# Optimization experiments

Hardware: AMD Instinct MI355X
Metric: run time of the kernel (lower is better)

## Reference

```python
import jax, jax.numpy as jnp
import numpy as np

D_MODEL = 1024
D_INNER = 2048        # expand=2
D_STATE = 128
NHEADS = 16           # d_inner / headdim
HEADDIM = 128
D_CONV = 4
D_XBC = D_INNER + 2 * D_STATE          # 2304 (ngroups=1)
D_IN_PROJ = 2 * D_INNER + 2 * D_STATE + NHEADS  # 4368
BATCH, SEQLEN = 2, 2048
EPS = 1e-5


def setup_inputs() -> dict:
    key = jax.random.key(0)
    ks = jax.random.split(key, 8)
    f = jnp.float32
    return {
        "x": jax.random.normal(ks[0], (BATCH, SEQLEN, D_MODEL), f),
        "ln_w": jnp.ones((D_MODEL,), f),
        "ln_b": jnp.zeros((D_MODEL,), f),
        "W_in": jax.random.normal(ks[1], (D_MODEL, D_IN_PROJ), f) * 0.02,
        "conv_w": jax.random.normal(ks[2], (D_XBC, D_CONV), f) * 0.2,
        "conv_b": jnp.zeros((D_XBC,), f),
        "dt_bias": jax.random.uniform(ks[3], (NHEADS,), f, -4.0, -2.0),
        "A_log": jnp.log(jax.random.uniform(ks[4], (NHEADS,), f, 1.0, 16.0)),
        "D": jnp.ones((NHEADS,), f),
        "rms_w": jnp.ones((D_INNER,), f),
        "W_out": jax.random.normal(ks[5], (D_INNER, D_MODEL), f) * 0.02,
    }


def _mamba_wrap(x, ln_w, ln_b, W_in, conv_w, conv_b, dt_bias, A_log, D, rms_w, W_out):
    B, L = x.shape[0], x.shape[1]
    # LayerNorm (pre-norm)
    mu = jnp.mean(x, -1, keepdims=True)
    var = jnp.mean(jnp.square(x - mu), -1, keepdims=True)
    xn = (x - mu) * jax.lax.rsqrt(var + EPS) * ln_w + ln_b
    # input projection -> z, xBC, dt
    zxbcdt = xn @ W_in                               # (B,L,4368)
    z = zxbcdt[..., :D_INNER]                        # (B,L,2048)
    xBC = zxbcdt[..., D_INNER:D_INNER + D_XBC]       # (B,L,2304)
    dt = jax.nn.softplus(zxbcdt[..., -NHEADS:] + dt_bias)  # (B,L,16)
    # causal depthwise conv1d (kernel 4), then SiLU
    xp = jnp.pad(xBC, ((0, 0), (D_CONV - 1, 0), (0, 0)))
    taps = jnp.stack([xp[:, k:k + L, :] for k in range(D_CONV)], axis=-1)  # (B,L,C,K)
    xBC = jax.nn.silu(jnp.einsum('blck,ck->blc', taps, conv_w) + conv_b)
    # split into SSM inputs
    xh = xBC[..., :D_INNER].reshape(B, L, NHEADS, HEADDIM)   # (B,L,H,P)
    Bm = xBC[..., D_INNER:D_INNER + D_STATE]                  # (B,L,N) ngroups=1
    Cm = xBC[..., D_INNER + D_STATE:]                         # (B,L,N)
    A = -jnp.exp(A_log)                                       # (H,)
    dA = jnp.exp(dt * A)                                      # (B,L,H)

    def step(state, inp):
        xt, dtt, dAt, Bt, Ct = inp  # (B,H,P),(B,H),(B,H),(B,N),(B,N)
        state = state * dAt[..., None, None] + (dtt[..., None] * xt)[..., None] * Bt[:, None, None, :]
        y = jnp.einsum('bhpn,bn->bhp', state, Ct)
        return state, y

    init = jnp.zeros((B, NHEADS, HEADDIM, D_STATE), x.dtype)
    xs = (xh.transpose(1, 0, 2, 3), dt.transpose(1, 0, 2), dA.transpose(1, 0, 2),
          Bm.transpose(1, 0, 2), Cm.transpose(1, 0, 2))
    _, ys = jax.lax.scan(step, init, xs)                      # (L,B,H,P)
    y = ys.transpose(1, 0, 2, 3) + D[None, None, :, None] * xh  # skip term
    y = y.reshape(B, L, D_INNER)
    # gated RMSNorm: rmsnorm(y * silu(z)) * weight
    y = y * jax.nn.silu(z)
    y = y * jax.lax.rsqrt(jnp.mean(y * y, -1, keepdims=True) + EPS) * rms_w
    # output projection + residual
    return x + y @ W_out


def reference(x, ln_w, ln_b, W_in, conv_w, conv_b, dt_bias, A_log, D, rms_w, W_out):
    return _mamba_wrap(x, ln_w, ln_b, W_in, conv_w, conv_b, dt_bias, A_log, D, rms_w, W_out)
```

## Files before the change

### kernel.cpp

```cpp
#include <hip/hip_runtime.h>

typedef unsigned short ushort_t;
typedef __attribute__((ext_vector_type(8))) unsigned short ushort8;
typedef __attribute__((ext_vector_type(4))) unsigned short ushortv4;
typedef __attribute__((ext_vector_type(8))) __bf16 bf16x8;
typedef __attribute__((ext_vector_type(4))) float f32x4;

#define BATCH   2
#define SEQLEN  2048
#define BL      4096
#define DMODEL  1024
#define DINNER  2048
#define DSTATE  128
#define NHEADS  16
#define DXBC    2304
#define DPROJ   4368
#define NPAD    4480
#define EPSF    1e-5f
#define QCH     128
#define NCH     16
#define BH      32

#define SWZ(row, colbyte) ((colbyte) ^ (((row) & 7) << 4))

#define GLDS(gp, lp) __builtin_amdgcn_global_load_lds( \
    (const __attribute__((address_space(1))) void*)(gp), \
    (__attribute__((address_space(3))) void*)(lp), 16, 0, 0)

__device__ __forceinline__ float bf2f(ushort_t h) {
    unsigned int u = ((unsigned int)h) << 16;
    float f; __builtin_memcpy(&f, &u, 4); return f;
}
__device__ __forceinline__ ushort_t f2bf(float f) {
    unsigned int u; __builtin_memcpy(&u, &f, 4);
    unsigned int r = u + 0x7fffu + ((u >> 16) & 1u);
    return (ushort_t)(r >> 16);
}
__device__ __forceinline__ float siluf(float x) { return x / (1.f + expf(-x)); }
__device__ __forceinline__ float softplusf(float x) { return (x > 20.f) ? x : log1pf(expf(x)); }

__global__ __launch_bounds__(256) void ln_kernel(const float* __restrict__ x,
        const float* __restrict__ w, const float* __restrict__ b, ushort_t* __restrict__ xn) {
    int r = blockIdx.x, t = threadIdx.x;
    const float* xr = x + (size_t)r * DMODEL;
    float4 v = *(const float4*)&xr[t * 4];
    float s  = v.x + v.y + v.z + v.w;
    float sq = v.x*v.x + v.y*v.y + v.z*v.z + v.w*v.w;
    __shared__ float red[8];
    #pragma unroll
    for (int m = 32; m >= 1; m >>= 1) { s += __shfl_xor(s, m, 64); sq += __shfl_xor(sq, m, 64); }
    int wv = t >> 6;
    if ((t & 63) == 0) { red[wv] = s; red[4 + wv] = sq; }
    __syncthreads();
    s  = red[0] + red[1] + red[2] + red[3];
    sq = red[4] + red[5] + red[6] + red[7];
    float mu  = s * (1.f / DMODEL);
    float var = sq * (1.f / DMODEL) - mu * mu;
    float inv = rsqrtf(var + EPSF);
    float4 wv4 = *(const float4*)&w[t * 4];
    float4 bv4 = *(const float4*)&b[t * 4];
    ushortv4 o;
    o[0] = f2bf((v.x - mu) * inv * wv4.x + bv4.x);
    o[1] = f2bf((v.y - mu) * inv * wv4.y + bv4.y);
    o[2] = f2bf((v.z - mu) * inv * wv4.z + bv4.z);
    o[3] = f2bf((v.w - mu) * inv * wv4.w + bv4.w);
    *(ushortv4*)&xn[(size_t)r * DMODEL + t * 4] = o;
}

__global__ __launch_bounds__(256) void transpose_cast(const float* __restrict__ W,
        ushort_t* __restrict__ WT, int K, int N) {
    __shared__ float tile[32][33];
    int n0 = blockIdx.x * 32, k0 = blockIdx.y * 32;
    int tx = threadIdx.x & 31, ty = threadIdx.x >> 5;
    #pragma unroll
    for (int i = 0; i < 32; i += 8) {
        int n = n0 + tx;
        tile[ty + i][tx] = (n < N) ? W[(size_t)(k0 + ty + i) * N + n] : 0.f;
    }
    __syncthreads();
    #pragma unroll
    for (int i = 0; i < 32; i += 8) {
        WT[(size_t)(n0 + ty + i) * K + k0 + tx] = f2bf(tile[tx][ty + i]);
    }
}

__global__ __launch_bounds__(256) void convw_tr(const float* __restrict__ w,
        float* __restrict__ wt) {
    int c = blockIdx.x * 256 + threadIdx.x;
    if (c < DXBC) {
        float4 v = *(const float4*)&w[c * 4];
        wt[0 * DXBC + c] = v.x;
        wt[1 * DXBC + c] = v.y;
        wt[2 * DXBC + c] = v.z;
        wt[3 * DXBC + c] = v.w;
    }
}

template <bool OUTBF>
__global__ __launch_bounds__(256) void gemm_bt(const ushort_t* __restrict__ A,
        const ushort_t* __restrict__ BT, void* __restrict__ Cv,
        const float* __restrict__ resid, int K, int ldc, int nbx) {
    const int tid = threadIdx.x;
    const int nwg = gridDim.x;
    const int cpx = nwg >> 3;
    const int lid = (blockIdx.x & 7) * cpx + (blockIdx.x >> 3);
    const int m0 = (lid / nbx) * 128, n0 = (lid % nbx) * 128;
    __shared__ ushort_t As[2][128 * 32];
    __shared__ ushort_t Bs[2][128 * 32];
    const int lane = tid & 63, wave = tid >> 6;
    const int wrow = wave * 32;
    const int srow = lane >> 2;
    const int selm = (lane & 3) * 8;
    const ushort_t* ag0 = A  + (size_t)(m0 + wrow + srow) * K + selm;
    const ushort_t* ag1 = ag0 + (size_t)16 * K;
    const ushort_t* bg0 = BT + (size_t)(n0 + wrow + srow) * K + selm;
    const ushort_t* bg1 = bg0 + (size_t)16 * K;
    const int wm = (wave >> 1) * 64, wn = (wave & 1) * 64;
    const int fr = lane & 15, ko = (lane >> 4) * 8;
    f32x4 acc[4][4];
    #pragma unroll
    for (int i = 0; i < 4; i++)
        #pragma unroll
        for (int j = 0; j < 4; j++) acc[i][j] = (f32x4){0.f, 0.f, 0.f, 0.f};
    GLDS(ag0, &As[0][wrow * 32]);
    GLDS(ag1, &As[0][(wrow + 16) * 32]);
    GLDS(bg0, &Bs[0][wrow * 32]);
    GLDS(bg1, &Bs[0][(wrow + 16) * 32]);
    __syncthreads();
    int cur = 0;
    for (int k0 = 0; k0 < K; k0 += 32) {
        const int nxt = cur ^ 1;
        if (k0 + 32 < K) {
            GLDS(ag0 + k0 + 32, &As[nxt][wrow * 32]);
            GLDS(ag1 + k0 + 32, &As[nxt][(wrow + 16) * 32]);
            GLDS(bg0 + k0 + 32, &Bs[nxt][wrow * 32]);
            GLDS(bg1 + k0 + 32, &Bs[nxt][(wrow + 16) * 32]);
        }
        bf16x8 af[4], bfr[4];
        #pragma unroll
        for (int i = 0; i < 4; i++) af[i]  = *(const bf16x8*)&As[cur][(wm + i * 16 + fr) * 32 + ko];
        #pragma unroll
        for (int j = 0; j < 4; j++) bfr[j] = *(const bf16x8*)&Bs[cur][(wn + j * 16 + fr) * 32 + ko];
        #pragma unroll
        for (int i = 0; i < 4; i++)
            #pragma unroll
            for (int j = 0; j < 4; j++)
                acc[i][j] = __builtin_amdgcn_mfma_f32_16x16x32_bf16(af[i], bfr[j], acc[i][j], 0, 0, 0);
        __syncthreads();
        cur = nxt;
    }
    const int r0 = (lane >> 4) * 4;
    #pragma unroll
    for (int i = 0; i < 4; i++)
        #pragma unroll
        for (int j = 0; j < 4; j++)
            #pragma unroll
            for (int r = 0; r < 4; r++) {
                int m = m0 + wm + i * 16 + r0 + r;
                int n = n0 + wn + j * 16 + fr;
                float v = acc[i][j][r];
                if (OUTBF) {
                    ((ushort_t*)Cv)[(size_t)m * ldc + n] = f2bf(v);
                } else {
                    if (resid) v += resid[(size_t)m * ldc + n];
                    ((float*)Cv)[(size_t)m * ldc + n] = v;
                }
            }
}

__global__ __launch_bounds__(256) void conv_kernel(const ushort_t* __restrict__ zxb,
        const float* __restrict__ wtr, const float* __restrict__ conv_b,
        const float* __restrict__ dt_bias, const float* __restrict__ A_log,
        ushort_t* __restrict__ xcv, ushort_t* __restrict__ Bcg, ushort_t* __restrict__ Ccg,
        float* __restrict__ dtv, float* __restrict__ dta) {
    int bid = blockIdx.x;
    int l = bid & (SEQLEN - 1);
    int tid = threadIdx.x;
    const ushort_t* rowp = zxb + (size_t)bid * NPAD;
    #pragma unroll 1
    for (int u = tid; u < DXBC / 8; u += 256) {
        int c0 = u * 8;
        float acc[8];
        {
            float4 b0 = *(const float4*)&conv_b[c0];
            float4 b1 = *(const float4*)&conv_b[c0 + 4];
            acc[0] = b0.x; acc[1] = b0.y; acc[2] = b0.z; acc[3] = b0.w;
            acc[4] = b1.x; acc[5] = b1.y; acc[6] = b1.z; acc[7] = b1.w;
        }
        #pragma unroll
        for (int k = 0; k < 4; k++) {
            int ll = l - 3 + k;
            if (ll >= 0) {
                ushort8 xv = *(const ushort8*)&rowp[(ptrdiff_t)(k - 3) * NPAD + DINNER + c0];
                float4 w0 = *(const float4*)&wtr[k * DXBC + c0];
                float4 w1 = *(const float4*)&wtr[k * DXBC + c0 + 4];
                acc[0] += bf2f((ushort_t)xv[0]) * w0.x;
                acc[1] += bf2f((ushort_t)xv[1]) * w0.y;
                acc[2] += bf2f((ushort_t)xv[2]) * w0.z;
                acc[3] += bf2f((ushort_t)xv[3]) * w0.w;
                acc[4] += bf2f((ushort_t)xv[4]) * w1.x;
                acc[5] += bf2f((ushort_t)xv[5]) * w1.y;
                acc[6] += bf2f((ushort_t)xv[6]) * w1.z;
                acc[7] += bf2f((ushort_t)xv[7]) * w1.w;
            }
        }
        ushort8 o;
        #pragma unroll
        for (int e = 0; e < 8; e++) o[e] = f2bf(siluf(acc[e]));
        if (c0 < DINNER)                *(ushort8*)&xcv[(size_t)bid * DINNER + c0] = o;
        else if (c0 < DINNER + DSTATE)  *(ushort8*)&Bcg[(size_t)bid * DSTATE + (c0 - DINNER)] = o;
        else                            *(ushort8*)&Ccg[(size_t)bid * DSTATE + (c0 - DINNER - DSTATE)] = o;
    }
    if (tid < NHEADS) {
        float raw = bf2f(rowp[DINNER + DXBC + tid]) + dt_bias[tid];
        float dt = softplusf(raw);
        float A = -expf(A_log[tid]);
        dtv[(size_t)bid * NHEADS + tid] = dt;
        dta[(size_t)bid * NHEADS + tid] = dt * A;
    }
}

__global__ __launch_bounds__(128) void cumsum_kernel(const float* __restrict__ dta,
        const float* __restrict__ dtv, float* __restrict__ cabuf, float* __restrict__ expca,
        float* __restrict__ wbuf, float* __restrict__ dtbuf, float* __restrict__ dtot) {
    const int c = blockIdx.x, h = blockIdx.y, b = blockIdx.z;
    const int bh = b * NHEADS + h;
    const int j = threadIdx.x;
    const size_t row = (size_t)b * SEQLEN + c * QCH + j;
    float v  = dta[row * NHEADS + h];
    float dt = dtv[row * NHEADS + h];
    float pv = v;
    #pragma unroll
    for (int off = 1; off < 64; off <<= 1) {
        float u = __shfl_up(pv, off, 64);
        if ((j & 63) >= off) pv += u;
    }
    __shared__ float wsum[2];
    if ((j & 63) == 63) wsum[j >> 6] = pv;
    __syncthreads();
    float tot = wsum[0] + wsum[1];
    if (j >= 64) pv += wsum[0];
    const size_t idx = ((size_t)bh * NCH + c) * QCH + j;
    cabuf[idx] = pv;
    expca[idx] = expf(pv);
    wbuf[idx]  = expf(tot - pv) * dt;
    dtbuf[idx] = dt;
    if (j == 0) dtot[bh * NCH + c] = expf(tot);
}

__global__ __launch_bounds__(256) void chunkstate_kernel(const ushort_t* __restrict__ xcv,
        const ushort_t* __restrict__ Bcg, const float* __restrict__ wbuf,
        ushort_t* __restrict__ states) {
    const int c = blockIdx.x, h = blockIdx.y, b = blockIdx.z;
    const int bh = b * NHEADS + h;
    const int tid = threadIdx.x;
    __shared__ ushort_t Xt[128 * 128];
    __shared__ ushort_t Bt[128 * 128];
    __shared__ float wsh[QCH];
    if (tid < QCH) wsh[tid] = wbuf[((size_t)bh * NCH + c) * QCH + tid];
    __syncthreads();
    const size_t row0 = (size_t)b * SEQLEN + c * QCH;
    {
        const int f = tid & 127;
        const int jh = (tid >> 7) * 64;
        const ushort_t* xsrc = xcv + (row0 + jh) * DINNER + h * 128 + f;
        const ushort_t* bsrc = Bcg + (row0 + jh) * DSTATE + f;
        char* xrow = (char*)Xt + f * 256;
        char* brow = (char*)Bt + f * 256;
        #pragma unroll 2
        for (int e8 = 0; e8 < 8; e8++) {
            ushort8 tx, tb;
            #pragma unroll
            for (int e = 0; e < 8; e++) {
                int j = e8 * 8 + e;
                tx[e] = xsrc[(size_t)j * DINNER];
                tb[e] = f2bf(bf2f(bsrc[(size_t)j * DSTATE]) * wsh[jh + j]);
            }
            int cb = (jh + e8 * 8) * 2;
            *(ushort8*)(xrow + SWZ(f, cb)) = tx;
            *(ushort8*)(brow + SWZ(f, cb)) = tb;
        }
    }
    __syncthreads();
    const int lane = tid & 63, wave = tid >> 6;
    const int wp = (wave >> 1) * 64, wn = (wave & 1) * 64;
    const int fr = lane & 15, ko = (lane >> 4) * 8;
    f32x4 acc[4][4];
    #pragma unroll
    for (int i = 0; i < 4; i++)
        #pragma unroll
        for (int j = 0; j < 4; j++) acc[i][j] = (f32x4){0.f, 0.f, 0.f, 0.f};
    for (int k0 = 0; k0 < 128; k0 += 32) {
        bf16x8 af[4], bfr[4];
        #pragma unroll
        for (int i = 0; i < 4; i++) {
            int rp = wp + i * 16 + fr;
            af[i] = *(const bf16x8*)((const char*)Xt + rp * 256 + SWZ(rp, (k0 + ko) * 2));
        }
        #pragma unroll
        for (int j = 0; j < 4; j++) {
            int rn = wn + j * 16 + fr;
            bfr[j] = *(const bf16x8*)((const char*)Bt + rn * 256 + SWZ(rn, (k0 + ko) * 2));
        }
        #pragma unroll
        for (int i = 0; i < 4; i++)
            #pragma unroll
            for (int j = 0; j < 4; j++)
                acc[i][j] = __builtin_amdgcn_mfma_f32_16x16x32_bf16(af[i], bfr[j], acc[i][j], 0, 0, 0);
    }
    const int r0 = (lane >> 4) * 4;
    ushort_t* outp = states + ((size_t)bh * NCH + c) * 16384;
    #pragma unroll
    for (int i = 0; i < 4; i++)
        #pragma unroll
        for (int j = 0; j < 4; j++)
            #pragma unroll
            for (int r = 0; r < 4; r++)
                outp[(wp + i * 16 + r0 + r) * 128 + wn + j * 16 + fr] = f2bf(acc[i][j][r]);
}

__global__ __launch_bounds__(256) void statescan_kernel(ushort_t* __restrict__ states,
        const float* __restrict__ dtot) {
    const int pseg = blockIdx.x, bh = blockIdx.y;
    const int tid = threadIdx.x;
    const int p = pseg * 8 + (tid >> 5);
    const int n4 = (tid & 31) * 4;
    ushort_t* base = states + (size_t)bh * NCH * 16384 + p * 128 + n4;
    const float* dtp = dtot + bh * NCH;
    float r0 = 0.f, r1 = 0.f, r2 = 0.f, r3 = 0.f;
    #pragma unroll 1
    for (int c = 0; c < NCH; c++) {
        ushortv4* ptr = (ushortv4*)(base + (size_t)c * 16384);
        ushortv4 cs = *ptr;
        ushortv4 o;
        o[0] = f2bf(r0); o[1] = f2bf(r1); o[2] = f2bf(r2); o[3] = f2bf(r3);
        *ptr = o;
        float d = dtp[c];
        r0 = r0 * d + bf2f(cs[0]);
        r1 = r1 * d + bf2f(cs[1]);
        r2 = r2 * d + bf2f(cs[2]);
        r3 = r3 * d + bf2f(cs[3]);
    }
}

__global__ __launch_bounds__(256) void chunkout_kernel(const ushort_t* __restrict__ xcv,
        const ushort_t* __restrict__ Bcg, const ushort_t* __restrict__ Ccg,
        const ushort_t* __restrict__ states, const float* __restrict__ cabuf,
        const float* __restrict__ expca, const float* __restrict__ dtbuf,
        const float* __restrict__ Dvec, ushort_t* __restrict__ yv) {
    const int c = blockIdx.x, h = blockIdx.y, b = blockIdx.z;
    const int bh = b * NHEADS + h;
    const int tid = threadIdx.x;
    __shared__ ushort_t R1[128 * 128];
    __shared__ ushort_t R2[128 * 128];
    __shared__ float cash[QCH], dtsh[QCH], exsh[QCH];
    const size_t aidx = ((size_t)bh * NCH + c) * QCH;
    if (tid < QCH) {
        cash[tid] = cabuf[aidx + tid];
        dtsh[tid] = dtbuf[aidx + tid];
        exsh[tid] = expca[aidx + tid];
    }
    const size_t row0 = (size_t)b * SEQLEN + c * QCH;
    {
        const ushort_t* sp = states + ((size_t)bh * NCH + c) * 16384;
        #pragma unroll
        for (int it = 0; it < 8; it++) {
            int g = tid + it * 256;
            int r = g >> 4, n8 = (g & 15) * 8;
            ushort8 vc = *(const ushort8*)&Ccg[(row0 + r) * DSTATE + n8];
            ushort8 vs = *(const ushort8*)&sp[r * 128 + n8];
            int cb = n8 * 2;
            *(ushort8*)((char*)R2 + r * 256 + SWZ(r, cb)) = vc;
            *(ushort8*)((char*)R1 + r * 256 + SWZ(r, cb)) = vs;
        }
    }
    __syncthreads();
    const int lane = tid & 63, wave = tid >> 6;
    const int fr = lane & 15, ko = (lane >> 4) * 8, r0 = (lane >> 4) * 4;
    const int wty = (wave >> 1) * 64, wpy = (wave & 1) * 64;
    f32x4 y_[4][4];
    #pragma unroll
    for (int i = 0; i < 4; i++)
        #pragma unroll
        for (int j = 0; j < 4; j++) y_[i][j] = (f32x4){0.f, 0.f, 0.f, 0.f};
    for (int k0 = 0; k0 < 128; k0 += 32) {
        bf16x8 af[4], bfr[4];
        #pragma unroll
        for (int i = 0; i < 4; i++) {
            int rt = wty + i * 16 + fr;
            af[i] = *(const bf16x8*)((const char*)R2 + rt * 256 + SWZ(rt, (k0 + ko) * 2));
        }
        #pragma unroll
        for (int j = 0; j < 4; j++) {
            int rp = wpy + j * 16 + fr;
            bfr[j] = *(const bf16x8*)((const char*)R1 + rp * 256 + SWZ(rp, (k0 + ko) * 2));
        }
        #pragma unroll
        for (int i = 0; i < 4; i++)
            #pragma unroll
            for (int j = 0; j < 4; j++)
                y_[i][j] = __builtin_amdgcn_mfma_f32_16x16x32_bf16(af[i], bfr[j], y_[i][j], 0, 0, 0);
    }
    #pragma unroll
    for (int i = 0; i < 4; i++)
        #pragma unroll
        for (int r = 0; r < 4; r++) {
            float sc = exsh[wty + i * 16 + r0 + r];
            #pragma unroll
            for (int j = 0; j < 4; j++) y_[i][j][r] *= sc;
        }
    __syncthreads();
    #pragma unroll
    for (int it = 0; it < 8; it++) {
        int g = tid + it * 256;
        int r = g >> 4, n8 = (g & 15) * 8;
        ushort8 vb = *(const ushort8*)&Bcg[(row0 + r) * DSTATE + n8];
        *(ushort8*)((char*)R1 + r * 256 + SWZ(r, n8 * 2)) = vb;
    }
    __syncthreads();
    const int wj = (wave >> 1) * 64, wt = (wave & 1) * 64;
    f32x4 g_[4][4];
    #pragma unroll
    for (int i = 0; i < 4; i++)
        #pragma unroll
        for (int t = 0; t < 4; t++) g_[i][t] = (f32x4){0.f, 0.f, 0.f, 0.f};
    if (!(wj == 64 && wt == 0)) {
        for (int k0 = 0; k0 < 128; k0 += 32) {
            bf16x8 af[4], bfr[4];
            #pragma unroll
            for (int i = 0; i < 4; i++) {
                int rj = wj + i * 16 + fr;
                af[i] = *(const bf16x8*)((const char*)R1 + rj * 256 + SWZ(rj, (k0 + ko) * 2));
            }
            #pragma unroll
            for (int t = 0; t < 4; t++) {
                int rt = wt + t * 16 + fr;
                bfr[t] = *(const bf16x8*)((const char*)R2 + rt * 256 + SWZ(rt, (k0 + ko) * 2));
            }
            #pragma unroll
            for (int i = 0; i < 4; i++)
                #pragma unroll
                for (int t = 0; t < 4; t++)
                    g_[i][t] = __builtin_amdgcn_mfma_f32_16x16x32_bf16(af[i], bfr[t], g_[i][t], 0, 0, 0);
        }
    }
    __syncthreads();
    {
        const float Dh = Dvec[h];
        #pragma unroll
        for (int i = 0; i < 4; i++) {
            #pragma unroll
            for (int t = 0; t < 4; t++) {
                int tt = wt + t * 16 + fr;
                int jj0 = wj + i * 16 + r0;
                ushortv4 pk;
                #pragma unroll
                for (int r = 0; r < 4; r++) {
                    int jj = jj0 + r;
                    float val = 0.f;
                    if (jj <= tt) {
                        val = g_[i][t][r] * expf(cash[tt] - cash[jj]) * dtsh[jj];
                        if (jj == tt) val += Dh;
                    }
                    pk[r] = f2bf(val);
                }
                *(ushortv4*)((char*)R1 + tt * 256 + SWZ(tt, jj0 * 2)) = pk;
            }
        }
        const int f = tid & 127;
        const int jh = (tid >> 7) * 64;
        const ushort_t* xsrc = xcv + (row0 + jh) * DINNER + h * 128 + f;
        char* xrow = (char*)R2 + f * 256;
        #pragma unroll 2
        for (int e8 = 0; e8 < 8; e8++) {
            ushort8 tx;
            #pragma unroll
            for (int e = 0; e < 8; e++) tx[e] = xsrc[(size_t)(e8 * 8 + e) * DINNER];
            int cb = (jh + e8 * 8) * 2;
            *(ushort8*)(xrow + SWZ(f, cb)) = tx;
        }
    }
    __syncthreads();
    const int kmax = wty + 64;
    for (int k0 = 0; k0 < kmax; k0 += 32) {
        bf16x8 af[4], bfr[4];
        #pragma unroll
        for (int i = 0; i < 4; i++) {
            int rt = wty + i * 16 + fr;
            af[i] = *(const bf16x8*)((const char*)R1 + rt * 256 + SWZ(rt, (k0 + ko) * 2));
        }
        #pragma unroll
        for (int j = 0; j < 4; j++) {
            int rp = wpy + j * 16 + fr;
            bfr[j] = *(const bf16x8*)((const char*)R2 + rp * 256 + SWZ(rp, (k0 + ko) * 2));
        }
        #pragma unroll
        for (int i = 0; i < 4; i++)
            #pragma unroll
            for (int j = 0; j < 4; j++)
                y_[i][j] = __builtin_amdgcn_mfma_f32_16x16x32_bf16(af[i], bfr[j], y_[i][j], 0, 0, 0);
    }
    #pragma unroll
    for (int i = 0; i < 4; i++)
        #pragma unroll
        for (int j = 0; j < 4; j++)
            #pragma unroll
            for (int r = 0; r < 4; r++) {
                int t = wty + i * 16 + r0 + r;
                int p = wpy + j * 16 + fr;
                yv[(row0 + t) * DINNER + h * 128 + p] = f2bf(y_[i][j][r]);
            }
}

__global__ __launch_bounds__(256) void gate_rms(const ushort_t* __restrict__ yv,
        const ushort_t* __restrict__ zxb, const float* __restrict__ rms_w,
        ushort_t* __restrict__ ynorm) {
    int r = blockIdx.x, t = threadIdx.x;
    const ushort_t* yr = yv + (size_t)r * DINNER;
    const ushort_t* zr = zxb + (size_t)r * NPAD;
    ushort8 y8 = *(const ushort8*)&yr[t * 8];
    ushort8 z8 = *(const ushort8*)&zr[t * 8];
    float g[8];
    #pragma unroll
    for (int j = 0; j < 8; j++)
        g[j] = bf2f((ushort_t)y8[j]) * siluf(bf2f((ushort_t)z8[j]));
    float sq = 0.f;
    #pragma unroll
    for (int j = 0; j < 8; j++) sq += g[j] * g[j];
    __shared__ float red[4];
    #pragma unroll
    for (int m = 32; m >= 1; m >>= 1) sq += __shfl_xor(sq, m, 64);
    int wv = t >> 6;
    if ((t & 63) == 0) red[wv] = sq;
    __syncthreads();
    sq = red[0] + red[1] + red[2] + red[3];
    float scale = rsqrtf(sq * (1.f / DINNER) + EPSF);
    float4 w0 = *(const float4*)&rms_w[t * 8];
    float4 w1 = *(const float4*)&rms_w[t * 8 + 4];
    ushort8 o;
    o[0] = f2bf(g[0] * scale * w0.x);
    o[1] = f2bf(g[1] * scale * w0.y);
    o[2] = f2bf(g[2] * scale * w0.z);
    o[3] = f2bf(g[3] * scale * w0.w);
    o[4] = f2bf(g[4] * scale * w1.x);
    o[5] = f2bf(g[5] * scale * w1.y);
    o[6] = f2bf(g[6] * scale * w1.z);
    o[7] = f2bf(g[7] * scale * w1.w);
    *(ushort8*)&ynorm[(size_t)r * DINNER + t * 8] = o;
}

extern "C" void kernel_launch(void* const* d_in, const int* in_sizes, int n_in,
                              void* d_out, int out_size, void* d_ws, size_t ws_size,
                              hipStream_t stream) {
    (void)in_sizes; (void)n_in; (void)out_size; (void)ws_size;
    const float* x       = (const float*)d_in[0];
    const float* ln_w    = (const float*)d_in[1];
    const float* ln_b    = (const float*)d_in[2];
    const float* W_in    = (const float*)d_in[3];
    const float* conv_w  = (const float*)d_in[4];
    const float* conv_b  = (const float*)d_in[5];
    const float* dt_bias = (const float*)d_in[6];
    const float* A_log   = (const float*)d_in[7];
    const float* Dvec    = (const float*)d_in[8];
    const float* rms_w   = (const float*)d_in[9];
    const float* W_out   = (const float*)d_in[10];
    float* out = (float*)d_out;

    char* ws = (char*)d_ws;
    size_t off = 0;
    auto alloc = [&](size_t bytes) -> void* {
        void* p = ws + off;
        off += (bytes + 255) & ~(size_t)255;
        return p;
    };
    ushort_t* xn    = (ushort_t*)alloc((size_t)BL * DMODEL * 2);
    ushort_t* WinT  = (ushort_t*)alloc((size_t)NPAD * DMODEL * 2);
    ushort_t* zxb   = (ushort_t*)alloc((size_t)BL * NPAD * 2);
    ushort_t* xcv   = (ushort_t*)alloc((size_t)BL * DINNER * 2);
    ushort_t* Bcg   = (ushort_t*)alloc((size_t)BL * DSTATE * 2);
    ushort_t* Ccg   = (ushort_t*)alloc((size_t)BL * DSTATE * 2);
    float*    dtv   = (float*)   alloc((size_t)BL * NHEADS * 4);
    float*    dta   = (float*)   alloc((size_t)BL * NHEADS * 4);
    ushort_t* yv    = (ushort_t*)alloc((size_t)BL * DINNER * 2);
    ushort_t* ynorm = (ushort_t*)alloc((size_t)BL * DINNER * 2);
    ushort_t* WoutT = (ushort_t*)alloc((size_t)DMODEL * DINNER * 2);
    float*    wtr   = (float*)   alloc((size_t)4 * DXBC * 4);
    float*    cabuf = (float*)   alloc((size_t)BH * NCH * QCH * 4);
    float*    expcb = (float*)   alloc((size_t)BH * NCH * QCH * 4);
    float*    wbuf  = (float*)   alloc((size_t)BH * NCH * QCH * 4);
    float*    dtbuf = (float*)   alloc((size_t)BH * NCH * QCH * 4);
    float*    dtot  = (float*)   alloc((size_t)BH * NCH * 4);
    ushort_t* states= (ushort_t*)alloc((size_t)BH * NCH * 16384 * 2);

    ln_kernel<<<BL, 256, 0, stream>>>(x, ln_w, ln_b, xn);
    transpose_cast<<<dim3(NPAD / 32, DMODEL / 32), 256, 0, stream>>>(W_in, WinT, DMODEL, DPROJ);
    transpose_cast<<<dim3(DMODEL / 32, DINNER / 32), 256, 0, stream>>>(W_out, WoutT, DINNER, DMODEL);
    convw_tr<<<(DXBC + 255) / 256, 256, 0, stream>>>(conv_w, wtr);
    gemm_bt<true><<<(NPAD / 128) * (BL / 128), 256, 0, stream>>>(xn, WinT, zxb, nullptr, DMODEL, NPAD, NPAD / 128);
    conv_kernel<<<BL, 256, 0, stream>>>(zxb, wtr, conv_b, dt_bias, A_log, xcv, Bcg, Ccg, dtv, dta);
    cumsum_kernel<<<dim3(NCH, NHEADS, BATCH), 128, 0, stream>>>(dta, dtv, cabuf, expcb, wbuf, dtbuf, dtot);
    chunkstate_kernel<<<dim3(NCH, NHEADS, BATCH), 256, 0, stream>>>(xcv, Bcg, wbuf, states);
    statescan_kernel<<<dim3(16, BH), 256, 0, stream>>>(states, dtot);
    chunkout_kernel<<<dim3(NCH, NHEADS, BATCH), 256, 0, stream>>>(xcv, Bcg, Ccg, states, cabuf, expcb, dtbuf, Dvec, yv);
    gate_rms<<<BL, 256, 0, stream>>>(yv, zxb, rms_w, ynorm);
    gemm_bt<false><<<(DMODEL / 128) * (BL / 128), 256, 0, stream>>>(ynorm, WoutT, out, x, DINNER, DMODEL, DMODEL / 128);
}
```

Baseline: 205.8 us.

## Triple-buffer GEMM LDS tiles with fine-grained vmcnt waits and XOR swizzle

The bf16 GEMM moves from double to triple buffering of the global-to-LDS tiles, prefetching two K-steps ahead. The full __syncthreads is replaced by explicit s_waitcnt vmcnt counts plus s_barrier, so loads for later tiles can stay in flight across iterations. The global source column is also XOR-swizzled by row, and the LDS reads un-swizzle to match, to cut LDS bank conflicts on the fragment reads. This costs extra LDS per block, which may lower occupancy, and relies on hand-counted vmcnt values being correct.

Measured after the change: 208.3 us. About the same (+1.2%).

```diff
diff --git a/kernel.cpp b/kernel.cpp
--- a/kernel.cpp
+++ b/kernel.cpp
@@ -105,12 +105,12 @@
     const int cpx = nwg >> 3;
     const int lid = (blockIdx.x & 7) * cpx + (blockIdx.x >> 3);
     const int m0 = (lid / nbx) * 128, n0 = (lid % nbx) * 128;
-    __shared__ ushort_t As[2][128 * 32];
-    __shared__ ushort_t Bs[2][128 * 32];
+    __shared__ ushort_t As[3][128 * 32];
+    __shared__ ushort_t Bs[3][128 * 32];
     const int lane = tid & 63, wave = tid >> 6;
     const int wrow = wave * 32;
     const int srow = lane >> 2;
-    const int selm = (lane & 3) * 8;
+    const int selm = ((lane & 3) ^ (srow & 3)) * 8;
     const ushort_t* ag0 = A  + (size_t)(m0 + wrow + srow) * K + selm;
     const ushort_t* ag1 = ag0 + (size_t)16 * K;
     const ushort_t* bg0 = BT + (size_t)(n0 + wrow + srow) * K + selm;
@@ -122,32 +122,49 @@
     for (int i = 0; i < 4; i++)
         #pragma unroll
         for (int j = 0; j < 4; j++) acc[i][j] = (f32x4){0.f, 0.f, 0.f, 0.f};
-    GLDS(ag0, &As[0][wrow * 32]);
-    GLDS(ag1, &As[0][(wrow + 16) * 32]);
-    GLDS(bg0, &Bs[0][wrow * 32]);
-    GLDS(bg1, &Bs[0][(wrow + 16) * 32]);
-    __syncthreads();
+    const int nt = K >> 5;
+    #pragma unroll
+    for (int t = 0; t < 3; t++) {
+        const size_t kof = (size_t)t * 32;
+        GLDS(ag0 + kof, &As[t][wrow * 32]);
+        GLDS(ag1 + kof, &As[t][(wrow + 16) * 32]);
+        GLDS(bg0 + kof, &Bs[t][wrow * 32]);
+        GLDS(bg1 + kof, &Bs[t][(wrow + 16) * 32]);
+    }
+    asm volatile("s_waitcnt vmcnt(8)" ::: "memory");
+    __builtin_amdgcn_s_barrier();
     int cur = 0;
-    for (int k0 = 0; k0 < K; k0 += 32) {
-        const int nxt = cur ^ 1;
-        if (k0 + 32 < K) {
-            GLDS(ag0 + k0 + 32, &As[nxt][wrow * 32]);
-            GLDS(ag1 + k0 + 32, &As[nxt][(wrow + 16) * 32]);
-            GLDS(bg0 + k0 + 32, &Bs[nxt][wrow * 32]);
-            GLDS(bg1 + k0 + 32, &Bs[nxt][(wrow + 16) * 32]);
+    for (int t = 0; t < nt; ++t) {
+        if (t + 2 < nt) {
+            int nb = cur + 2; if (nb >= 3) nb -= 3;
+            const size_t kof = (size_t)(t + 2) * 32;
+            GLDS(ag0 + kof, &As[nb][wrow * 32]);
+            GLDS(ag1 + kof, &As[nb][(wrow + 16) * 32]);
+            GLDS(bg0 + kof, &Bs[nb][wrow * 32]);
+            GLDS(bg1 + kof, &Bs[nb][(wrow + 16) * 32]);
         }
         bf16x8 af[4], bfr[4];
         #pragma unroll
-        for (int i = 0; i < 4; i++) af[i]  = *(const bf16x8*)&As[cur][(wm + i * 16 + fr) * 32 + ko];
-        #pragma unroll
-        for (int j = 0; j < 4; j++) bfr[j] = *(const bf16x8*)&Bs[cur][(wn + j * 16 + fr) * 32 + ko];
+        for (int i = 0; i < 4; i++) {
+            int row = wm + i * 16 + fr;
+            af[i] = *(const bf16x8*)((const char*)&As[cur][0] + row * 64
+                                     + ((ko * 2) ^ ((row & 3) << 4)));
+        }
+        #pragma unroll
+        for (int j = 0; j < 4; j++) {
+            int row = wn + j * 16 + fr;
+            bfr[j] = *(const bf16x8*)((const char*)&Bs[cur][0] + row * 64
+                                      + ((ko * 2) ^ ((row & 3) << 4)));
+        }
         #pragma unroll
         for (int i = 0; i < 4; i++)
             #pragma unroll
             for (int j = 0; j < 4; j++)
                 acc[i][j] = __builtin_amdgcn_mfma_f32_16x16x32_bf16(af[i], bfr[j], acc[i][j], 0, 0, 0);
-        __syncthreads();
-        cur = nxt;
+        if (t + 2 < nt) asm volatile("s_waitcnt vmcnt(4)" ::: "memory");
+        else            asm volatile("s_waitcnt vmcnt(0)" ::: "memory");
+        __builtin_amdgcn_s_barrier();
+        cur = (cur == 2) ? 0 : cur + 1;
     }
     const int r0 = (lane >> 4) * 4;
     #pragma unroll
```
